# Kernel optimization log

Hardware: AMD Instinct MI355X
Metric: run time of the kernel (lower is better)

Reference implementation:

```python
import jax, jax.numpy as jnp
import numpy as np
import math

IN_CH = 256
EMBED = 128


def setup_inputs() -> dict:
    key = jax.random.key(0)
    k1, k2, k3, k4, k5 = jax.random.split(key, 5)
    N, C, H, W = 4, IN_CH, 64, 64
    x = jax.random.normal(k1, (N, C, H, W), dtype=jnp.float32)
    # conv1x1 weights stored as [out_ch, in_ch] (kernel is 1x1)
    W_qkv = jax.random.normal(k2, (3 * EMBED, C), dtype=jnp.float32) * (1.0 / math.sqrt(C))
    b_qkv = jax.random.normal(k3, (3 * EMBED,), dtype=jnp.float32) * 0.01
    W_out = jax.random.normal(k4, (C, EMBED), dtype=jnp.float32) * (1.0 / math.sqrt(EMBED))
    b_out = jax.random.normal(k5, (C,), dtype=jnp.float32) * 0.01
    return {"x": x, "W_qkv": W_qkv, "b_qkv": b_qkv, "W_out": W_out, "b_out": b_out}


def reference(x, W_qkv, b_qkv, W_out, b_out):
    N, C, H, W = x.shape
    E = EMBED
    HW = H * W
    # conv1x1 QKV projection: (N, 3E, H, W)
    qkv = jnp.einsum('nchw,oc->nohw', x, W_qkv) + b_qkv[None, :, None, None]
    # faithful RAW C-order reshape (N, 3E, H, W) -> (N, HW, 3E), as in torch .reshape
    qkv = qkv.reshape(N, HW, 3 * E)
    q, k, v = jnp.split(qkv, 3, axis=-1)  # each (N, HW, E)
    # scores scaled by 1/sqrt(H*W), softmax over dim=-2 (columns)
    scores = jnp.einsum('nid,njd->nij', q, k) / math.sqrt(HW)
    soft = jax.nn.softmax(scores, axis=-2)
    out = jnp.einsum('nij,njd->nid', soft, v)  # (N, HW, E)
    # faithful RAW C-order reshape (N, HW, E) -> (N, E, H, W)
    out = out.reshape(N, E, H, W)
    # conv1x1 output projection
    y = jnp.einsum('nehw,ce->nchw', out, W_out) + b_out[None, :, None, None]
    return y
```

## Files before the change

### kernel.cpp

```cpp
#include <hip/hip_runtime.h>
#include <hip/hip_bf16.h>


typedef short bfrag __attribute__((ext_vector_type(8)));
typedef float ffrag __attribute__((ext_vector_type(4)));
typedef unsigned short us4 __attribute__((ext_vector_type(4)));
#define MFMA(a,b,c) __builtin_amdgcn_mfma_f32_16x16x32_bf16((a),(b),(c),0,0,0)

__device__ __forceinline__ unsigned short f2bf(float f){
  union { float f; unsigned u; } v; v.f = f;
  unsigned r = v.u + 0x7fffu + ((v.u >> 16) & 1u);
  return (unsigned short)(r >> 16);
}
__device__ __forceinline__ float bf2f(unsigned short h){
  union { unsigned u; float f; } v; v.u = ((unsigned)h) << 16; return v.f;
}
__device__ __forceinline__ unsigned bfpack(float a, float b){
  return (unsigned)f2bf(a) | ((unsigned)f2bf(b) << 16);
}

__global__ __launch_bounds__(256) void k_qkv(const float* __restrict__ x, const float* __restrict__ Wq,
                                             const float* __restrict__ bq, unsigned short* __restrict__ qkv){
  constexpr int LD = 136;
  __shared__ __align__(16) unsigned short As[128*LD];
  __shared__ __align__(16) unsigned short Bs[64*LD];
  char* BsB = (char*)Bs;
  const int o0 = blockIdx.x*128, h0 = blockIdx.y*64, n = blockIdx.z;
  const int t = threadIdx.x, w = t>>6, lane = t&63, lr = lane&15, q4 = lane>>4;
  ffrag acc[8] = {};
  for (int kh = 0; kh < 2; ++kh) {
    __syncthreads();
    #pragma unroll
    for (int r=0;r<8;++r){
      int pi = t + 256*r; int o = pi>>4, seg = pi&15;
      const float* wsrc = Wq + (size_t)(o0+o)*256 + kh*128 + seg*8;
      float4 w0 = *(const float4*)(wsrc);
      float4 w1 = *(const float4*)(wsrc+4);
      us4 lo, hv;
      lo.x=f2bf(w0.x); lo.y=f2bf(w0.y); lo.z=f2bf(w0.z); lo.w=f2bf(w0.w);
      hv.x=f2bf(w1.x); hv.y=f2bf(w1.y); hv.z=f2bf(w1.z); hv.w=f2bf(w1.w);
      *(us4*)&As[o*LD + seg*8]     = lo;
      *(us4*)&As[o*LD + seg*8 + 4] = hv;
    }
    #pragma unroll
    for (int r=0;r<8;++r){
      int idx = t + 256*r; int cl = idx>>4, h4 = idx&15;
      float4 v = *(const float4*)(x + (size_t)(n*256 + kh*128 + cl)*4096 + h0 + h4*4);
      float vv[4] = {v.x, v.y, v.z, v.w};
      #pragma unroll
      for (int u=0;u<4;++u){
        int row = h4*4+u;
        *(unsigned short*)(BsB + row*272 + ((2*cl) ^ (((row>>3)&7)<<4))) = f2bf(vv[u]);
      }
    }
    __syncthreads();
    const int arow = w*16+lr;
    const int akey = ((arow>>3)&7)<<4;
    #pragma unroll
    for (int kk=0;kk<4;++kk){
      bfrag a = *(const bfrag*)(BsB + arow*272 + ((kk*64 + q4*16) ^ akey));
      #pragma unroll
      for (int ot=0;ot<8;++ot){
        bfrag b = *(const bfrag*)&As[(ot*16+lr)*LD + kk*32 + q4*8];
        acc[ot] = MFMA(a,b,acc[ot]);
      }
    }
  }
  size_t base = (size_t)n*384*4096;
  #pragma unroll
  for (int ot=0;ot<8;++ot){
    int o  = o0 + ot*16 + lr;
    float bias = bq[o];
    int hw = h0 + w*16 + q4*4;
    us4 pk;
    pk.x = f2bf(acc[ot][0] + bias); pk.y = f2bf(acc[ot][1] + bias);
    pk.z = f2bf(acc[ot][2] + bias); pk.w = f2bf(acc[ot][3] + bias);
    *(us4*)(qkv + base + (size_t)o*4096 + hw) = pk;
  }
}

__global__ __launch_bounds__(256, 2) void k_stats(const unsigned short* __restrict__ qkv,
                                                  float* __restrict__ zp){
  constexpr int LD = 136;
  __shared__ __align__(16) unsigned short Qs[2][64*LD];
  const int j0 = blockIdx.x*256, ic = blockIdx.y, n = blockIdx.z;
  const int t = threadIdx.x, w = t>>6, lane = t&63, lr = lane&15, q4 = lane>>4;
  size_t base = (size_t)n*384*4096;
  bfrag kf[4][4];
  #pragma unroll
  for (int js=0; js<4; ++js){
    const unsigned short* krow = qkv + base + (size_t)(j0 + w*64 + js*16 + lr)*384 + 128;
    #pragma unroll
    for (int kk=0;kk<4;++kk) kf[js][kk] = *(const bfrag*)(krow + kk*32 + q4*8);
  }
  const int il = t>>4, seg = t&15;
  {
    const int i0 = (ic<<9);
    #pragma unroll
    for (int r=0;r<4;++r)
      *(uint4*)&Qs[0][(il+16*r)*LD + seg*8] =
        *(const uint4*)(qkv + base + (size_t)(i0+il+16*r)*384 + seg*8);
  }
  __syncthreads();
  float Zc[16] = {};
  const float inv64 = 0.015625f;
  for (int rnd=0; rnd<8; ++rnd){
    const int cur = rnd&1;
    uint4 qr[4];
    if (rnd<7){
      const int i1 = (ic<<9) + (rnd+1)*64;
      #pragma unroll
      for (int r=0;r<4;++r)
        qr[r] = *(const uint4*)(qkv + base + (size_t)(i1+il+16*r)*384 + seg*8);
    }
    const unsigned short* qs = Qs[cur];
    #pragma unroll
    for (int it=0; it<4; ++it){
      bfrag qb[4];
      #pragma unroll
      for (int kk=0;kk<4;++kk) qb[kk] = *(const bfrag*)&qs[(it*16+lr)*LD + kk*32 + q4*8];
      #pragma unroll
      for (int js=0; js<4; ++js){
        ffrag s = {};
        #pragma unroll
        for (int kk=0;kk<4;++kk) s = MFMA(kf[js][kk], qb[kk], s);
        #pragma unroll
        for (int r=0;r<4;++r) Zc[js*4+r] += __expf(s[r]*inv64);
      }
    }
    if (rnd<7){
      #pragma unroll
      for (int r=0;r<4;++r) *(uint4*)&Qs[cur^1][(il+16*r)*LD + seg*8] = qr[r];
      __syncthreads();
    }
  }
  #pragma unroll
  for (int v=0; v<16; ++v){
    float z = Zc[v];
    z += __shfl_xor(z, 1); z += __shfl_xor(z, 2);
    z += __shfl_xor(z, 4); z += __shfl_xor(z, 8);
    Zc[v] = z;
  }
  if (lr == 0){
    int jb = j0 + w*64;
    float* zrow = zp + (size_t)((n<<3)+ic)*4096;
    #pragma unroll
    for (int js=0; js<4; ++js)
      #pragma unroll
      for (int r=0;r<4;++r)
        zrow[jb + js*16 + q4*4 + r] = Zc[js*4+r];
  }
}

__global__ __launch_bounds__(256) void k_vtrans(const unsigned short* __restrict__ qkv,
                                                const float* __restrict__ zp,
                                                unsigned short* __restrict__ vt){
  constexpr int LD = 136;
  __shared__ __align__(16) unsigned short T[64*LD];
  __shared__ float invZ[64];
  const int p0 = blockIdx.x*64, n = blockIdx.y;
  const int t = threadIdx.x;
  size_t base = (size_t)n*384*4096;
  #pragma unroll
  for (int r=0;r<4;++r){
    int pi = t + 256*r; int pl = pi>>4, seg = pi&15;
    *(uint4*)&T[pl*LD + seg*8] = *(const uint4*)(qkv + base + (size_t)(p0+pl)*384 + 256 + seg*8);
  }
  if (t < 64){
    float Z = 0.f;
    #pragma unroll
    for (int c=0;c<8;++c) Z += zp[(size_t)((n<<3)+c)*4096 + p0 + t];
    invZ[t] = 1.0f / Z;
  }
  __syncthreads();
  unsigned* vt32 = (unsigned*)(vt + (size_t)n*128*4096);
  #pragma unroll
  for (int r=0;r<16;++r){
    int pi = t + 256*r;
    int d = pi>>5, k = pi&31;
    float lo = bf2f(T[(2*k)*LD + d])   * invZ[2*k];
    float hi = bf2f(T[(2*k+1)*LD + d]) * invZ[2*k+1];
    vt32[(size_t)d*2048 + (p0>>1) + k] = bfpack(lo, hi);
  }
}

__global__ __launch_bounds__(256, 2) void k_attn(const unsigned short* __restrict__ qkv,
                                                 const unsigned short* __restrict__ vtg_all,
                                                 unsigned short* __restrict__ part){
  constexpr int LDK = 136, LDV = 72;
  __shared__ __align__(16) unsigned short Ks[2][64*LDK];
  __shared__ __align__(16) unsigned short Vt[2][128*LDV];
  const int i0 = blockIdx.x*128, jh = blockIdx.y, n = blockIdx.z;
  const int t = threadIdx.x, w = t>>6, lane = t&63, lr = lane&15, q4 = lane>>4;
  size_t base = (size_t)n*384*4096;
  const unsigned short* vtg = vtg_all + (size_t)n*128*4096;
  bfrag qf[2][4];
  #pragma unroll
  for (int isub=0;isub<2;++isub){
    const unsigned short* qrow = qkv + base + (size_t)(i0 + w*32 + isub*16 + lr)*384;
    #pragma unroll
    for (int kk=0;kk<4;++kk) qf[isub][kk] = *(const bfrag*)(qrow + kk*32 + q4*8);
  }
  ffrag acc[8][2] = {};
  const float inv64 = 0.015625f;

  const int jl_k = t>>4, seg_k = t&15;
  const int d_v  = t>>3, c_v  = t&7;
  const int sl0 = lr + 16*((2*q4)   & 3);
  const int sl1 = lr + 16*((2*q4+1) & 3);

  {
    const int j0 = jh*1024;
    #pragma unroll
    for (int r=0;r<4;++r)
      *(uint4*)&Ks[0][(jl_k+16*r)*LDK + seg_k*8] =
        *(const uint4*)(qkv + base + (size_t)(j0 + jl_k + 16*r)*384 + 128 + seg_k*8);
    #pragma unroll
    for (int r=0;r<4;++r)
      *(uint4*)&Vt[0][(d_v+32*r)*LDV + c_v*8] =
        *(const uint4*)(vtg + (size_t)(d_v + 32*r)*4096 + j0 + c_v*8);
  }
  __syncthreads();

  for (int it=0; it<16; ++it){
    const int cur = it & 1;
    uint4 kr[4], vr[4];
    if (it < 15){
      const int jn = jh*1024 + (it+1)*64;
      #pragma unroll
      for (int r=0;r<4;++r)
        kr[r] = *(const uint4*)(qkv + base + (size_t)(jn + jl_k + 16*r)*384 + 128 + seg_k*8);
      #pragma unroll
      for (int r=0;r<4;++r)
        vr[r] = *(const uint4*)(vtg + (size_t)(d_v + 32*r)*4096 + jn + c_v*8);
    }
    unsigned pk[4][2][2];
    #pragma unroll
    for (int jt=0;jt<4;++jt){
      bfrag kf[4];
      #pragma unroll
      for (int kk=0;kk<4;++kk) kf[kk] = *(const bfrag*)&Ks[cur][(jt*16+lr)*LDK + kk*32 + q4*8];
      #pragma unroll
      for (int isub=0;isub<2;++isub){
        ffrag s = {};
        #pragma unroll
        for (int kk=0;kk<4;++kk) s = MFMA(kf[kk], qf[isub][kk], s);
        pk[jt][isub][0] = bfpack(__expf(s[0]*inv64), __expf(s[1]*inv64));
        pk[jt][isub][1] = bfpack(__expf(s[2]*inv64), __expf(s[3]*inv64));
      }
    }
    #pragma unroll
    for (int jk=0;jk<2;++jk){
      union { bfrag b; uint4 u; } pf0, pf1;
      unsigned v0[4], v1[4];
      #pragma unroll
      for (int m=0;m<4;++m){
        const int sl = (m<2) ? sl0 : sl1;
        unsigned a0 = __shfl(pk[2*jk  ][0][m&1], sl);
        unsigned b0 = __shfl(pk[2*jk+1][0][m&1], sl);
        v0[m] = (q4 >= 2) ? b0 : a0;
        unsigned a1 = __shfl(pk[2*jk  ][1][m&1], sl);
        unsigned b1 = __shfl(pk[2*jk+1][1][m&1], sl);
        v1[m] = (q4 >= 2) ? b1 : a1;
      }
      pf0.u = make_uint4(v0[0],v0[1],v0[2],v0[3]);
      pf1.u = make_uint4(v1[0],v1[1],v1[2],v1[3]);
      #pragma unroll
      for (int dt=0;dt<8;++dt){
        bfrag af = *(const bfrag*)&Vt[cur][(dt*16+lr)*LDV + jk*32 + q4*8];
        acc[dt][0] = MFMA(af, pf0.b, acc[dt][0]);
        acc[dt][1] = MFMA(af, pf1.b, acc[dt][1]);
      }
    }
    if (it < 15){
      #pragma unroll
      for (int r=0;r<4;++r) *(uint4*)&Ks[cur^1][(jl_k+16*r)*LDK + seg_k*8] = kr[r];
      #pragma unroll
      for (int r=0;r<4;++r) *(uint4*)&Vt[cur^1][(d_v+32*r)*LDV + c_v*8] = vr[r];
      __syncthreads();
    }
  }
  unsigned short* po = part + (size_t)(jh*4+n)*524288;
  #pragma unroll
  for (int isub=0;isub<2;++isub){
    const int i = i0 + w*32 + isub*16 + lr;
    #pragma unroll
    for (int dt=0;dt<8;++dt){
      us4 pko;
      pko.x = f2bf(acc[dt][isub][0]); pko.y = f2bf(acc[dt][isub][1]);
      pko.z = f2bf(acc[dt][isub][2]); pko.w = f2bf(acc[dt][isub][3]);
      *(us4*)(po + (size_t)i*128 + dt*16 + q4*4) = pko;
    }
  }
}

__global__ __launch_bounds__(256) void k_oproj(const unsigned short* __restrict__ part,
                                               const float* __restrict__ Wo,
                                               const float* __restrict__ bo, float* __restrict__ y){
  constexpr int LD = 136;
  __shared__ __align__(16) unsigned short As[128*LD];
  __shared__ __align__(16) unsigned short Rt[64*LD];
  char* RtB = (char*)Rt;
  const int c0 = blockIdx.x*128, h0 = blockIdx.y*64, n = blockIdx.z;
  const int t = threadIdx.x, w = t>>6, lane = t&63, lr = lane&15, q4 = lane>>4;
  #pragma unroll
  for (int r=0;r<8;++r){
    int pi = t + 256*r; int cl = pi>>4, seg = pi&15;
    const float* wsrc = Wo + (size_t)(c0+cl)*128 + seg*8;
    float4 w0 = *(const float4*)(wsrc);
    float4 w1 = *(const float4*)(wsrc+4);
    us4 lo, hv;
    lo.x=f2bf(w0.x); lo.y=f2bf(w0.y); lo.z=f2bf(w0.z); lo.w=f2bf(w0.w);
    hv.x=f2bf(w1.x); hv.y=f2bf(w1.y); hv.z=f2bf(w1.z); hv.w=f2bf(w1.w);
    *(us4*)&As[cl*LD + seg*8]     = lo;
    *(us4*)&As[cl*LD + seg*8 + 4] = hv;
  }
  #pragma unroll
  for (int r=0;r<4;++r){
    int pi = t + 256*r; int e = pi>>3, h8 = pi&7;
    size_t f = (size_t)e*4096 + h0 + h8*8;
    float a[8] = {};
    #pragma unroll
    for (int s=0;s<4;++s){
      uint4 u = *(const uint4*)(part + (size_t)(s*4+n)*524288 + f);
      a[0] += bf2f((unsigned short)(u.x & 0xffffu)); a[1] += bf2f((unsigned short)(u.x >> 16));
      a[2] += bf2f((unsigned short)(u.y & 0xffffu)); a[3] += bf2f((unsigned short)(u.y >> 16));
      a[4] += bf2f((unsigned short)(u.z & 0xffffu)); a[5] += bf2f((unsigned short)(u.z >> 16));
      a[6] += bf2f((unsigned short)(u.w & 0xffffu)); a[7] += bf2f((unsigned short)(u.w >> 16));
    }
    #pragma unroll
    for (int u2=0;u2<8;++u2){
      int row = h8*8+u2;
      *(unsigned short*)(RtB + row*272 + ((2*e) ^ (((row>>3)&7)<<4))) = f2bf(a[u2]);
    }
  }
  __syncthreads();
  ffrag acc[8] = {};
  const int arow = w*16+lr;
  const int akey = ((arow>>3)&7)<<4;
  #pragma unroll
  for (int kk=0;kk<4;++kk){
    bfrag a = *(const bfrag*)(RtB + arow*272 + ((kk*64 + q4*16) ^ akey));
    #pragma unroll
    for (int cs=0;cs<8;++cs){
      bfrag b = *(const bfrag*)&As[(cs*16+lr)*LD + kk*32 + q4*8];
      acc[cs] = MFMA(a,b,acc[cs]);
    }
  }
  #pragma unroll
  for (int cs=0;cs<8;++cs){
    int c = c0 + cs*16 + lr;
    float bias = bo[c];
    float4 v4 = { acc[cs][0]+bias, acc[cs][1]+bias, acc[cs][2]+bias, acc[cs][3]+bias };
    *(float4*)(y + ((size_t)n*256 + c)*4096 + h0 + w*16 + q4*4) = v4;
  }
}

extern "C" void kernel_launch(void* const* d_in, const int* in_sizes, int n_in,
                              void* d_out, int out_size, void* d_ws, size_t ws_size,
                              hipStream_t stream){
  const float* x  = (const float*)d_in[0];
  const float* Wq = (const float*)d_in[1];
  const float* bq = (const float*)d_in[2];
  const float* Wo = (const float*)d_in[3];
  const float* bo = (const float*)d_in[4];
  float* y = (float*)d_out;
  char* ws = (char*)d_ws;
  unsigned short* qkv  = (unsigned short*)(ws + 0);
  unsigned short* vtg  = (unsigned short*)(ws + 12582912);
  float* zp   = (float*)(ws + 17039360);
  unsigned short* part = (unsigned short*)(ws + 17629184);

  k_qkv   <<<dim3(3,64,4),  256, 0, stream>>>(x, Wq, bq, qkv);
  k_stats <<<dim3(16,8,4),  256, 0, stream>>>(qkv, zp);
  k_vtrans<<<dim3(64,4),    256, 0, stream>>>(qkv, zp, vtg);
  k_attn  <<<dim3(32,4,4),  256, 0, stream>>>(qkv, vtg, part);
  k_oproj <<<dim3(2,64,4),  256, 0, stream>>>(part, Wo, bo, y);
}
```

Before: 182.2 us.

## Fuse five attention stages into one persistent kernel with grid barriers

Replaces five separate kernel launches (QKV projection, softmax column stats, V transpose/normalize, attention, output projection) with a single persistent kernel of 512 blocks. The stages are separated by atomic-counter grid barriers, and a memset resets the counter before launch. This removes per-launch overhead and the idle gaps between kernels. In exchange it needs all 512 blocks to be co-resident, with 2 blocks per CU on 256 CUs and 70KB of shared memory each, or it deadlocks. It also loses occupancy on the lighter stages and adds barrier spin cost.

```diff
diff --git a/kernel.cpp b/kernel.cpp
--- a/kernel.cpp
+++ b/kernel.cpp
@@ -19,340 +19,349 @@
   return (unsigned)f2bf(a) | ((unsigned)f2bf(b) << 16);
 }
 
-__global__ __launch_bounds__(256) void k_qkv(const float* __restrict__ x, const float* __restrict__ Wq,
-                                             const float* __restrict__ bq, unsigned short* __restrict__ qkv){
+__device__ __forceinline__ void grid_barrier(unsigned* bar, unsigned target){
+  __syncthreads();
+  __threadfence();
+  if (threadIdx.x == 0){
+    atomicAdd(bar, 1u);
+    while (__hip_atomic_load(bar, __ATOMIC_RELAXED, __HIP_MEMORY_SCOPE_AGENT) < target)
+      __builtin_amdgcn_s_sleep(2);
+  }
+  __syncthreads();
+  __threadfence();
+}
+
+__global__ __launch_bounds__(256, 2) void k_fused(
+    const float* __restrict__ x,  const float* __restrict__ Wq, const float* __restrict__ bq,
+    const float* __restrict__ Wo, const float* __restrict__ bo,
+    unsigned short* __restrict__ qkv, unsigned short* __restrict__ vtg_all,
+    float* __restrict__ zp, unsigned short* __restrict__ part, float* __restrict__ y,
+    unsigned* __restrict__ bar)
+{
+  __shared__ __align__(16) char smem[71680];
+  const int bid = blockIdx.x;
+  const int t = threadIdx.x, w = t>>6, lane = t&63, lr = lane&15, q4 = lane>>4;
   constexpr int LD = 136;
-  __shared__ __align__(16) unsigned short As[128*LD];
-  __shared__ __align__(16) unsigned short Bs[64*LD];
-  char* BsB = (char*)Bs;
-  const int o0 = blockIdx.x*128, h0 = blockIdx.y*64, n = blockIdx.z;
-  const int t = threadIdx.x, w = t>>6, lane = t&63, lr = lane&15, q4 = lane>>4;
-  ffrag acc[8] = {};
-  for (int kh = 0; kh < 2; ++kh) {
+  const float inv64 = 0.015625f;
+
+  {
+    unsigned short* As = (unsigned short*)smem;
+    char* BsB = smem + 34816;
+    for (int v = bid; v < 768; v += 512){
+      const int o0=(v%3)*128, h0=((v/3)&63)*64, n=v/192;
+      ffrag acc[8] = {};
+      for (int kh = 0; kh < 2; ++kh) {
+        __syncthreads();
+        #pragma unroll
+        for (int r=0;r<8;++r){
+          int pi = t + 256*r; int o = pi>>4, seg = pi&15;
+          const float* wsrc = Wq + (size_t)(o0+o)*256 + kh*128 + seg*8;
+          float4 w0 = *(const float4*)(wsrc);
+          float4 w1 = *(const float4*)(wsrc+4);
+          us4 lo, hv;
+          lo.x=f2bf(w0.x); lo.y=f2bf(w0.y); lo.z=f2bf(w0.z); lo.w=f2bf(w0.w);
+          hv.x=f2bf(w1.x); hv.y=f2bf(w1.y); hv.z=f2bf(w1.z); hv.w=f2bf(w1.w);
+          *(us4*)&As[o*LD + seg*8]     = lo;
+          *(us4*)&As[o*LD + seg*8 + 4] = hv;
+        }
+        #pragma unroll
+        for (int r=0;r<8;++r){
+          int idx = t + 256*r; int cl = idx>>4, h4 = idx&15;
+          float4 v4 = *(const float4*)(x + (size_t)(n*256 + kh*128 + cl)*4096 + h0 + h4*4);
+          float vv[4] = {v4.x, v4.y, v4.z, v4.w};
+          #pragma unroll
+          for (int u=0;u<4;++u){
+            int row = h4*4+u;
+            *(unsigned short*)(BsB + row*272 + ((2*cl) ^ (((row>>3)&7)<<4))) = f2bf(vv[u]);
+          }
+        }
+        __syncthreads();
+        const int arow = w*16+lr;
+        const int akey = ((arow>>3)&7)<<4;
+        #pragma unroll
+        for (int kk=0;kk<4;++kk){
+          bfrag a = *(const bfrag*)(BsB + arow*272 + ((kk*64 + q4*16) ^ akey));
+          #pragma unroll
+          for (int ot=0;ot<8;++ot){
+            bfrag b = *(const bfrag*)&As[(ot*16+lr)*LD + kk*32 + q4*8];
+            acc[ot] = MFMA(a,b,acc[ot]);
+          }
+        }
+      }
+      size_t base = (size_t)n*384*4096;
+      #pragma unroll
+      for (int ot=0;ot<8;++ot){
+        int o  = o0 + ot*16 + lr;
+        float bias = bq[o];
+        int hw = h0 + w*16 + q4*4;
+        us4 pk;
+        pk.x = f2bf(acc[ot][0] + bias); pk.y = f2bf(acc[ot][1] + bias);
+        pk.z = f2bf(acc[ot][2] + bias); pk.w = f2bf(acc[ot][3] + bias);
+        *(us4*)(qkv + base + (size_t)o*4096 + hw) = pk;
+      }
+    }
+  }
+  grid_barrier(bar, 512u);
+
+  {
+    unsigned short (*Qs)[64*LD] = (unsigned short(*)[64*LD])smem;
+    const int j0 = (bid&15)*256, ic = (bid>>4)&7, n = bid>>7;
+    size_t base = (size_t)n*384*4096;
+    bfrag kf[4][4];
+    #pragma unroll
+    for (int js=0; js<4; ++js){
+      const unsigned short* krow = qkv + base + (size_t)(j0 + w*64 + js*16 + lr)*384 + 128;
+      #pragma unroll
+      for (int kk=0;kk<4;++kk) kf[js][kk] = *(const bfrag*)(krow + kk*32 + q4*8);
+    }
+    const int il = t>>4, seg = t&15;
+    {
+      const int i0 = (ic<<9);
+      #pragma unroll
+      for (int r=0;r<4;++r)
+        *(uint4*)&Qs[0][(il+16*r)*LD + seg*8] =
+          *(const uint4*)(qkv + base + (size_t)(i0+il+16*r)*384 + seg*8);
+    }
     __syncthreads();
+    float Zc[16] = {};
+    for (int rnd=0; rnd<8; ++rnd){
+      const int cur = rnd&1;
+      uint4 qr[4];
+      if (rnd<7){
+        const int i1 = (ic<<9) + (rnd+1)*64;
+        #pragma unroll
+        for (int r=0;r<4;++r)
+          qr[r] = *(const uint4*)(qkv + base + (size_t)(i1+il+16*r)*384 + seg*8);
+      }
+      const unsigned short* qs = Qs[cur];
+      #pragma unroll
+      for (int it=0; it<4; ++it){
+        bfrag qb[4];
+        #pragma unroll
+        for (int kk=0;kk<4;++kk) qb[kk] = *(const bfrag*)&qs[(it*16+lr)*LD + kk*32 + q4*8];
+        #pragma unroll
+        for (int js=0; js<4; ++js){
+          ffrag s = {};
+          #pragma unroll
+          for (int kk=0;kk<4;++kk) s = MFMA(kf[js][kk], qb[kk], s);
+          #pragma unroll
+          for (int r=0;r<4;++r) Zc[js*4+r] += __expf(s[r]*inv64);
+        }
+      }
+      if (rnd<7){
+        #pragma unroll
+        for (int r=0;r<4;++r) *(uint4*)&Qs[cur^1][(il+16*r)*LD + seg*8] = qr[r];
+        __syncthreads();
+      }
+    }
+    #pragma unroll
+    for (int v=0; v<16; ++v){
+      float z = Zc[v];
+      z += __shfl_xor(z, 1); z += __shfl_xor(z, 2);
+      z += __shfl_xor(z, 4); z += __shfl_xor(z, 8);
+      Zc[v] = z;
+    }
+    if (lr == 0){
+      int jb = j0 + w*64;
+      float* zrow = zp + (size_t)((n<<3)+ic)*4096;
+      #pragma unroll
+      for (int js=0; js<4; ++js)
+        #pragma unroll
+        for (int r=0;r<4;++r)
+          zrow[jb + js*16 + q4*4 + r] = Zc[js*4+r];
+    }
+  }
+  grid_barrier(bar, 1024u);
+
+  if (bid < 256){
+    unsigned short* T = (unsigned short*)smem;
+    float* invZ = (float*)(smem + 17408);
+    const int p0 = (bid&63)*64, n = bid>>6;
+    size_t base = (size_t)n*384*4096;
+    #pragma unroll
+    for (int r=0;r<4;++r){
+      int pi = t + 256*r; int pl = pi>>4, seg = pi&15;
+      *(uint4*)&T[pl*LD + seg*8] = *(const uint4*)(qkv + base + (size_t)(p0+pl)*384 + 256 + seg*8);
+    }
+    if (t < 64){
+      float Z = 0.f;
+      #pragma unroll
+      for (int c=0;c<8;++c) Z += zp[(size_t)((n<<3)+c)*4096 + p0 + t];
+      invZ[t] = 1.0f / Z;
+    }
+    __syncthreads();
+    unsigned* vt32 = (unsigned*)(vtg_all + (size_t)n*128*4096);
+    #pragma unroll
+    for (int r=0;r<16;++r){
+      int pi = t + 256*r;
+      int d = pi>>5, k = pi&31;
+      float lo = bf2f(T[(2*k)*LD + d])   * invZ[2*k];
+      float hi = bf2f(T[(2*k+1)*LD + d]) * invZ[2*k+1];
+      vt32[(size_t)d*2048 + (p0>>1) + k] = bfpack(lo, hi);
+    }
+  }
+  grid_barrier(bar, 1536u);
+
+  {
+    constexpr int LDK = 136, LDV = 72;
+    unsigned short (*Ks)[64*LDK] = (unsigned short(*)[64*LDK])smem;
+    unsigned short (*Vt)[128*LDV] = (unsigned short(*)[128*LDV])(smem + 34816);
+    const int i0 = (bid&31)*128, jh = (bid>>5)&3, n = bid>>7;
+    size_t base = (size_t)n*384*4096;
+    const unsigned short* vtg = vtg_all + (size_t)n*128*4096;
+    bfrag qf[2][4];
+    #pragma unroll
+    for (int isub=0;isub<2;++isub){
+      const unsigned short* qrow = qkv + base + (size_t)(i0 + w*32 + isub*16 + lr)*384;
+      #pragma unroll
+      for (int kk=0;kk<4;++kk) qf[isub][kk] = *(const bfrag*)(qrow + kk*32 + q4*8);
+    }
+    ffrag acc[8][2] = {};
+    const int jl_k = t>>4, seg_k = t&15;
+    const int d_v  = t>>3, c_v  = t&7;
+    const int sl0 = lr + 16*((2*q4)   & 3);
+    const int sl1 = lr + 16*((2*q4+1) & 3);
+    {
+      const int j0 = jh*1024;
+      #pragma unroll
+      for (int r=0;r<4;++r)
+        *(uint4*)&Ks[0][(jl_k+16*r)*LDK + seg_k*8] =
+          *(const uint4*)(qkv + base + (size_t)(j0 + jl_k + 16*r)*384 + 128 + seg_k*8);
+      #pragma unroll
+      for (int r=0;r<4;++r)
+        *(uint4*)&Vt[0][(d_v+32*r)*LDV + c_v*8] =
+          *(const uint4*)(vtg + (size_t)(d_v + 32*r)*4096 + j0 + c_v*8);
+    }
+    __syncthreads();
+
+    for (int it=0; it<16; ++it){
+      const int cur = it & 1;
+      uint4 kr[4], vr[4];
+      if (it < 15){
+        const int jn = jh*1024 + (it+1)*64;
+        #pragma unroll
+        for (int r=0;r<4;++r)
+          kr[r] = *(const uint4*)(qkv + base + (size_t)(jn + jl_k + 16*r)*384 + 128 + seg_k*8);
+        #pragma unroll
+        for (int r=0;r<4;++r)
+          vr[r] = *(const uint4*)(vtg + (size_t)(d_v + 32*r)*4096 + jn + c_v*8);
+      }
+      unsigned pk[4][2][2];
+      #pragma unroll
+      for (int jt=0;jt<4;++jt){
+        bfrag kf[4];
+        #pragma unroll
+        for (int kk=0;kk<4;++kk) kf[kk] = *(const bfrag*)&Ks[cur][(jt*16+lr)*LDK + kk*32 + q4*8];
+        #pragma unroll
+        for (int isub=0;isub<2;++isub){
+          ffrag s = {};
+          #pragma unroll
+          for (int kk=0;kk<4;++kk) s = MFMA(kf[kk], qf[isub][kk], s);
+          pk[jt][isub][0] = bfpack(__expf(s[0]*inv64), __expf(s[1]*inv64));
+          pk[jt][isub][1] = bfpack(__expf(s[2]*inv64), __expf(s[3]*inv64));
+        }
+      }
+      #pragma unroll
+      for (int jk=0;jk<2;++jk){
+        union { bfrag b; uint4 u; } pf0, pf1;
+        unsigned v0[4], v1[4];
+        #pragma unroll
+        for (int m=0;m<4;++m){
+          const int sl = (m<2) ? sl0 : sl1;
+          unsigned a0 = __shfl(pk[2*jk  ][0][m&1], sl);
+          unsigned b0 = __shfl(pk[2*jk+1][0][m&1], sl);
+          v0[m] = (q4 >= 2) ? b0 : a0;
+          unsigned a1 = __shfl(pk[2*jk  ][1][m&1], sl);
+          unsigned b1 = __shfl(pk[2*jk+1][1][m&1], sl);
+          v1[m] = (q4 >= 2) ? b1 : a1;
+        }
+        pf0.u = make_uint4(v0[0],v0[1],v0[2],v0[3]);
+        pf1.u = make_uint4(v1[0],v1[1],v1[2],v1[3]);
+        #pragma unroll
+        for (int dt=0;dt<8;++dt){
+          bfrag af = *(const bfrag*)&Vt[cur][(dt*16+lr)*LDV + jk*32 + q4*8];
+          acc[dt][0] = MFMA(af, pf0.b, acc[dt][0]);
+          acc[dt][1] = MFMA(af, pf1.b, acc[dt][1]);
+        }
+      }
+      if (it < 15){
+        #pragma unroll
+        for (int r=0;r<4;++r) *(uint4*)&Ks[cur^1][(jl_k+16*r)*LDK + seg_k*8] = kr[r];
+        #pragma unroll
+        for (int r=0;r<4;++r) *(uint4*)&Vt[cur^1][(d_v+32*r)*LDV + c_v*8] = vr[r];
+        __syncthreads();
+      }
+    }
+    unsigned short* po = part + (size_t)(jh*4+n)*524288;
+    #pragma unroll
+    for (int isub=0;isub<2;++isub){
+      const int i = i0 + w*32 + isub*16 + lr;
+      #pragma unroll
+      for (int dt=0;dt<8;++dt){
+        us4 pko;
+        pko.x = f2bf(acc[dt][isub][0]); pko.y = f2bf(acc[dt][isub][1]);
+        pko.z = f2bf(acc[dt][isub][2]); pko.w = f2bf(acc[dt][isub][3]);
+        *(us4*)(po + (size_t)i*128 + dt*16 + q4*4) = pko;
+      }
+    }
+  }
+  grid_barrier(bar, 2048u);
+
+  {
+    unsigned short* As = (unsigned short*)smem;
+    char* RtB = smem + 34816;
+    const int c0 = (bid&1)*128, h0 = ((bid>>1)&63)*64, n = bid>>7;
     #pragma unroll
     for (int r=0;r<8;++r){
-      int pi = t + 256*r; int o = pi>>4, seg = pi&15;
-      const float* wsrc = Wq + (size_t)(o0+o)*256 + kh*128 + seg*8;
+      int pi = t + 256*r; int cl = pi>>4, seg = pi&15;
+      const float* wsrc = Wo + (size_t)(c0+cl)*128 + seg*8;
       float4 w0 = *(const float4*)(wsrc);
       float4 w1 = *(const float4*)(wsrc+4);
       us4 lo, hv;
       lo.x=f2bf(w0.x); lo.y=f2bf(w0.y); lo.z=f2bf(w0.z); lo.w=f2bf(w0.w);
       hv.x=f2bf(w1.x); hv.y=f2bf(w1.y); hv.z=f2bf(w1.z); hv.w=f2bf(w1.w);
-      *(us4*)&As[o*LD + seg*8]     = lo;
-      *(us4*)&As[o*LD + seg*8 + 4] = hv;
-    }
-    #pragma unroll
-    for (int r=0;r<8;++r){
-      int idx = t + 256*r; int cl = idx>>4, h4 = idx&15;
-      float4 v = *(const float4*)(x + (size_t)(n*256 + kh*128 + cl)*4096 + h0 + h4*4);
-      float vv[4] = {v.x, v.y, v.z, v.w};
-      #pragma unroll
-      for (int u=0;u<4;++u){
-        int row = h4*4+u;
-        *(unsigned short*)(BsB + row*272 + ((2*cl) ^ (((row>>3)&7)<<4))) = f2bf(vv[u]);
+      *(us4*)&As[cl*LD + seg*8]     = lo;
+      *(us4*)&As[cl*LD + seg*8 + 4] = hv;
+    }
+    #pragma unroll
+    for (int r=0;r<4;++r){
+      int pi = t + 256*r; int e = pi>>3, h8 = pi&7;
+      size_t f = (size_t)e*4096 + h0 + h8*8;
+      float a[8] = {};
+      #pragma unroll
+      for (int s=0;s<4;++s){
+        uint4 u = *(const uint4*)(part + (size_t)(s*4+n)*524288 + f);
+        a[0] += bf2f((unsigned short)(u.x & 0xffffu)); a[1] += bf2f((unsigned short)(u.x >> 16));
+        a[2] += bf2f((unsigned short)(u.y & 0xffffu)); a[3] += bf2f((unsigned short)(u.y >> 16));
+        a[4] += bf2f((unsigned short)(u.z & 0xffffu)); a[5] += bf2f((unsigned short)(u.z >> 16));
+        a[6] += bf2f((unsigned short)(u.w & 0xffffu)); a[7] += bf2f((unsigned short)(u.w >> 16));
+      }
+      #pragma unroll
+      for (int u2=0;u2<8;++u2){
+        int row = h8*8+u2;
+        *(unsigned short*)(RtB + row*272 + ((2*e) ^ (((row>>3)&7)<<4))) = f2bf(a[u2]);
       }
     }
     __syncthreads();
+    ffrag acc[8] = {};
     const int arow = w*16+lr;
     const int akey = ((arow>>3)&7)<<4;
     #pragma unroll
     for (int kk=0;kk<4;++kk){
-      bfrag a = *(const bfrag*)(BsB + arow*272 + ((kk*64 + q4*16) ^ akey));
-      #pragma unroll
-      for (int ot=0;ot<8;++ot){
-        bfrag b = *(const bfrag*)&As[(ot*16+lr)*LD + kk*32 + q4*8];
-        acc[ot] = MFMA(a,b,acc[ot]);
-      }
-    }
-  }
-  size_t base = (size_t)n*384*4096;
-  #pragma unroll
-  for (int ot=0;ot<8;++ot){
-    int o  = o0 + ot*16 + lr;
-    float bias = bq[o];
-    int hw = h0 + w*16 + q4*4;
-    us4 pk;
-    pk.x = f2bf(acc[ot][0] + bias); pk.y = f2bf(acc[ot][1] + bias);
-    pk.z = f2bf(acc[ot][2] + bias); pk.w = f2bf(acc[ot][3] + bias);
-    *(us4*)(qkv + base + (size_t)o*4096 + hw) = pk;
-  }
-}
-
-__global__ __launch_bounds__(256, 2) void k_stats(const unsigned short* __restrict__ qkv,
-                                                  float* __restrict__ zp){
-  constexpr int LD = 136;
-  __shared__ __align__(16) unsigned short Qs[2][64*LD];
-  const int j0 = blockIdx.x*256, ic = blockIdx.y, n = blockIdx.z;
-  const int t = threadIdx.x, w = t>>6, lane = t&63, lr = lane&15, q4 = lane>>4;
-  size_t base = (size_t)n*384*4096;
-  bfrag kf[4][4];
-  #pragma unroll
-  for (int js=0; js<4; ++js){
-    const unsigned short* krow = qkv + base + (size_t)(j0 + w*64 + js*16 + lr)*384 + 128;
-    #pragma unroll
-    for (int kk=0;kk<4;++kk) kf[js][kk] = *(const bfrag*)(krow + kk*32 + q4*8);
-  }
-  const int il = t>>4, seg = t&15;
-  {
-    const int i0 = (ic<<9);
-    #pragma unroll
-    for (int r=0;r<4;++r)
-      *(uint4*)&Qs[0][(il+16*r)*LD + seg*8] =
-        *(const uint4*)(qkv + base + (size_t)(i0+il+16*r)*384 + seg*8);
-  }
-  __syncthreads();
-  float Zc[16] = {};
-  const float inv64 = 0.015625f;
-  for (int rnd=0; rnd<8; ++rnd){
-    const int cur = rnd&1;
-    uint4 qr[4];
-    if (rnd<7){
-      const int i1 = (ic<<9) + (rnd+1)*64;
-      #pragma unroll
-      for (int r=0;r<4;++r)
-        qr[r] = *(const uint4*)(qkv + base + (size_t)(i1+il+16*r)*384 + seg*8);
-    }
-    const unsigned short* qs = Qs[cur];
-    #pragma unroll
-    for (int it=0; it<4; ++it){
-      bfrag qb[4];
-      #pragma unroll
-      for (int kk=0;kk<4;++kk) qb[kk] = *(const bfrag*)&qs[(it*16+lr)*LD + kk*32 + q4*8];
-      #pragma unroll
-      for (int js=0; js<4; ++js){
-        ffrag s = {};
-        #pragma unroll
-        for (int kk=0;kk<4;++kk) s = MFMA(kf[js][kk], qb[kk], s);
-        #pragma unroll
-        for (int r=0;r<4;++r) Zc[js*4+r] += __expf(s[r]*inv64);
-      }
-    }
-    if (rnd<7){
-      #pragma unroll
-      for (int r=0;r<4;++r) *(uint4*)&Qs[cur^1][(il+16*r)*LD + seg*8] = qr[r];
-      __syncthreads();
-    }
-  }
-  #pragma unroll
-  for (int v=0; v<16; ++v){
-    float z = Zc[v];
-    z += __shfl_xor(z, 1); z += __shfl_xor(z, 2);
-    z += __shfl_xor(z, 4); z += __shfl_xor(z, 8);
-    Zc[v] = z;
-  }
-  if (lr == 0){
-    int jb = j0 + w*64;
-    float* zrow = zp + (size_t)((n<<3)+ic)*4096;
-    #pragma unroll
-    for (int js=0; js<4; ++js)
-      #pragma unroll
-      for (int r=0;r<4;++r)
-        zrow[jb + js*16 + q4*4 + r] = Zc[js*4+r];
-  }
-}
-
-__global__ __launch_bounds__(256) void k_vtrans(const unsigned short* __restrict__ qkv,
-                                                const float* __restrict__ zp,
-                                                unsigned short* __restrict__ vt){
-  constexpr int LD = 136;
-  __shared__ __align__(16) unsigned short T[64*LD];
-  __shared__ float invZ[64];
-  const int p0 = blockIdx.x*64, n = blockIdx.y;
-  const int t = threadIdx.x;
-  size_t base = (size_t)n*384*4096;
-  #pragma unroll
-  for (int r=0;r<4;++r){
-    int pi = t + 256*r; int pl = pi>>4, seg = pi&15;
-    *(uint4*)&T[pl*LD + seg*8] = *(const uint4*)(qkv + base + (size_t)(p0+pl)*384 + 256 + seg*8);
-  }
-  if (t < 64){
-    float Z = 0.f;
-    #pragma unroll
-    for (int c=0;c<8;++c) Z += zp[(size_t)((n<<3)+c)*4096 + p0 + t];
-    invZ[t] = 1.0f / Z;
-  }
-  __syncthreads();
-  unsigned* vt32 = (unsigned*)(vt + (size_t)n*128*4096);
-  #pragma unroll
-  for (int r=0;r<16;++r){
-    int pi = t + 256*r;
-    int d = pi>>5, k = pi&31;
-    float lo = bf2f(T[(2*k)*LD + d])   * invZ[2*k];
-    float hi = bf2f(T[(2*k+1)*LD + d]) * invZ[2*k+1];
-    vt32[(size_t)d*2048 + (p0>>1) + k] = bfpack(lo, hi);
-  }
-}
-
-__global__ __launch_bounds__(256, 2) void k_attn(const unsigned short* __restrict__ qkv,
-                                                 const unsigned short* __restrict__ vtg_all,
-                                                 unsigned short* __restrict__ part){
-  constexpr int LDK = 136, LDV = 72;
-  __shared__ __align__(16) unsigned short Ks[2][64*LDK];
-  __shared__ __align__(16) unsigned short Vt[2][128*LDV];
-  const int i0 = blockIdx.x*128, jh = blockIdx.y, n = blockIdx.z;
-  const int t = threadIdx.x, w = t>>6, lane = t&63, lr = lane&15, q4 = lane>>4;
-  size_t base = (size_t)n*384*4096;
-  const unsigned short* vtg = vtg_all + (size_t)n*128*4096;
-  bfrag qf[2][4];
-  #pragma unroll
-  for (int isub=0;isub<2;++isub){
-    const unsigned short* qrow = qkv + base + (size_t)(i0 + w*32 + isub*16 + lr)*384;
-    #pragma unroll
-    for (int kk=0;kk<4;++kk) qf[isub][kk] = *(const bfrag*)(qrow + kk*32 + q4*8);
-  }
-  ffrag acc[8][2] = {};
-  const float inv64 = 0.015625f;
-
-  const int jl_k = t>>4, seg_k = t&15;
-  const int d_v  = t>>3, c_v  = t&7;
-  const int sl0 = lr + 16*((2*q4)   & 3);
-  const int sl1 = lr + 16*((2*q4+1) & 3);
-
-  {
-    const int j0 = jh*1024;
-    #pragma unroll
-    for (int r=0;r<4;++r)
-      *(uint4*)&Ks[0][(jl_k+16*r)*LDK + seg_k*8] =
-        *(const uint4*)(qkv + base + (size_t)(j0 + jl_k + 16*r)*384 + 128 + seg_k*8);
-    #pragma unroll
-    for (int r=0;r<4;++r)
-      *(uint4*)&Vt[0][(d_v+32*r)*LDV + c_v*8] =
-        *(const uint4*)(vtg + (size_t)(d_v + 32*r)*4096 + j0 + c_v*8);
-  }
-  __syncthreads();
-
-  for (int it=0; it<16; ++it){
-    const int cur = it & 1;
-    uint4 kr[4], vr[4];
-    if (it < 15){
-      const int jn = jh*1024 + (it+1)*64;
-      #pragma unroll
-      for (int r=0;r<4;++r)
-        kr[r] = *(const uint4*)(qkv + base + (size_t)(jn + jl_k + 16*r)*384 + 128 + seg_k*8);
-      #pragma unroll
-      for (int r=0;r<4;++r)
-        vr[r] = *(const uint4*)(vtg + (size_t)(d_v + 32*r)*4096 + jn + c_v*8);
-    }
-    unsigned pk[4][2][2];
-    #pragma unroll
-    for (int jt=0;jt<4;++jt){
-      bfrag kf[4];
-      #pragma unroll
-      for (int kk=0;kk<4;++kk) kf[kk] = *(const bfrag*)&Ks[cur][(jt*16+lr)*LDK + kk*32 + q4*8];
-      #pragma unroll
-      for (int isub=0;isub<2;++isub){
-        ffrag s = {};
-        #pragma unroll
-        for (int kk=0;kk<4;++kk) s = MFMA(kf[kk], qf[isub][kk], s);
-        pk[jt][isub][0] = bfpack(__expf(s[0]*inv64), __expf(s[1]*inv64));
-        pk[jt][isub][1] = bfpack(__expf(s[2]*inv64), __expf(s[3]*inv64));
-      }
-    }
-    #pragma unroll
-    for (int jk=0;jk<2;++jk){
-      union { bfrag b; uint4 u; } pf0, pf1;
-      unsigned v0[4], v1[4];
-      #pragma unroll
-      for (int m=0;m<4;++m){
-        const int sl = (m<2) ? sl0 : sl1;
-        unsigned a0 = __shfl(pk[2*jk  ][0][m&1], sl);
-        unsigned b0 = __shfl(pk[2*jk+1][0][m&1], sl);
-        v0[m] = (q4 >= 2) ? b0 : a0;
-        unsigned a1 = __shfl(pk[2*jk  ][1][m&1], sl);
-        unsigned b1 = __shfl(pk[2*jk+1][1][m&1], sl);
-        v1[m] = (q4 >= 2) ? b1 : a1;
-      }
-      pf0.u = make_uint4(v0[0],v0[1],v0[2],v0[3]);
-      pf1.u = make_uint4(v1[0],v1[1],v1[2],v1[3]);
-      #pragma unroll
-      for (int dt=0;dt<8;++dt){
-        bfrag af = *(const bfrag*)&Vt[cur][(dt*16+lr)*LDV + jk*32 + q4*8];
-        acc[dt][0] = MFMA(af, pf0.b, acc[dt][0]);
-        acc[dt][1] = MFMA(af, pf1.b, acc[dt][1]);
-      }
-    }
-    if (it < 15){
-      #pragma unroll
-      for (int r=0;r<4;++r) *(uint4*)&Ks[cur^1][(jl_k+16*r)*LDK + seg_k*8] = kr[r];
-      #pragma unroll
-      for (int r=0;r<4;++r) *(uint4*)&Vt[cur^1][(d_v+32*r)*LDV + c_v*8] = vr[r];
-      __syncthreads();
-    }
-  }
-  unsigned short* po = part + (size_t)(jh*4+n)*524288;
-  #pragma unroll
-  for (int isub=0;isub<2;++isub){
-    const int i = i0 + w*32 + isub*16 + lr;
-    #pragma unroll
-    for (int dt=0;dt<8;++dt){
-      us4 pko;
-      pko.x = f2bf(acc[dt][isub][0]); pko.y = f2bf(acc[dt][isub][1]);
-      pko.z = f2bf(acc[dt][isub][2]); pko.w = f2bf(acc[dt][isub][3]);
-      *(us4*)(po + (size_t)i*128 + dt*16 + q4*4) = pko;
-    }
-  }
-}
-
-__global__ __launch_bounds__(256) void k_oproj(const unsigned short* __restrict__ part,
-                                               const float* __restrict__ Wo,
-                                               const float* __restrict__ bo, float* __restrict__ y){
-  constexpr int LD = 136;
-  __shared__ __align__(16) unsigned short As[128*LD];
-  __shared__ __align__(16) unsigned short Rt[64*LD];
-  char* RtB = (char*)Rt;
-  const int c0 = blockIdx.x*128, h0 = blockIdx.y*64, n = blockIdx.z;
-  const int t = threadIdx.x, w = t>>6, lane = t&63, lr = lane&15, q4 = lane>>4;
-  #pragma unroll
-  for (int r=0;r<8;++r){
-    int pi = t + 256*r; int cl = pi>>4, seg = pi&15;
-    const float* wsrc = Wo + (size_t)(c0+cl)*128 + seg*8;
-    float4 w0 = *(const float4*)(wsrc);
-    float4 w1 = *(const float4*)(wsrc+4);
-    us4 lo, hv;
-    lo.x=f2bf(w0.x); lo.y=f2bf(w0.y); lo.z=f2bf(w0.z); lo.w=f2bf(w0.w);
-    hv.x=f2bf(w1.x); hv.y=f2bf(w1.y); hv.z=f2bf(w1.z); hv.w=f2bf(w1.w);
-    *(us4*)&As[cl*LD + seg*8]     = lo;
-    *(us4*)&As[cl*LD + seg*8 + 4] = hv;
-  }
-  #pragma unroll
-  for (int r=0;r<4;++r){
-    int pi = t + 256*r; int e = pi>>3, h8 = pi&7;
-    size_t f = (size_t)e*4096 + h0 + h8*8;
-    float a[8] = {};
-    #pragma unroll
-    for (int s=0;s<4;++s){
-      uint4 u = *(const uint4*)(part + (size_t)(s*4+n)*524288 + f);
-      a[0] += bf2f((unsigned short)(u.x & 0xffffu)); a[1] += bf2f((unsigned short)(u.x >> 16));
-      a[2] += bf2f((unsigned short)(u.y & 0xffffu)); a[3] += bf2f((unsigned short)(u.y >> 16));
-      a[4] += bf2f((unsigned short)(u.z & 0xffffu)); a[5] += bf2f((unsigned short)(u.z >> 16));
-      a[6] += bf2f((unsigned short)(u.w & 0xffffu)); a[7] += bf2f((unsigned short)(u.w >> 16));
-    }
-    #pragma unroll
-    for (int u2=0;u2<8;++u2){
-      int row = h8*8+u2;
-      *(unsigned short*)(RtB + row*272 + ((2*e) ^ (((row>>3)&7)<<4))) = f2bf(a[u2]);
-    }
-  }
-  __syncthreads();
-  ffrag acc[8] = {};
-  const int arow = w*16+lr;
-  const int akey = ((arow>>3)&7)<<4;
-  #pragma unroll
-  for (int kk=0;kk<4;++kk){
-    bfrag a = *(const bfrag*)(RtB + arow*272 + ((kk*64 + q4*16) ^ akey));
+      bfrag a = *(const bfrag*)(RtB + arow*272 + ((kk*64 + q4*16) ^ akey));
+      #pragma unroll
+      for (int cs=0;cs<8;++cs){
+        bfrag b = *(const bfrag*)&As[(cs*16+lr)*LD + kk*32 + q4*8];
+        acc[cs] = MFMA(a,b,acc[cs]);
+      }
+    }
     #pragma unroll
     for (int cs=0;cs<8;++cs){
-      bfrag b = *(const bfrag*)&As[(cs*16+lr)*LD + kk*32 + q4*8];
-      acc[cs] = MFMA(a,b,acc[cs]);
-    }
-  }
-  #pragma unroll
-  for (int cs=0;cs<8;++cs){
-    int c = c0 + cs*16 + lr;
-    float bias = bo[c];
-    float4 v4 = { acc[cs][0]+bias, acc[cs][1]+bias, acc[cs][2]+bias, acc[cs][3]+bias };
-    *(float4*)(y + ((size_t)n*256 + c)*4096 + h0 + w*16 + q4*4) = v4;
+      int c = c0 + cs*16 + lr;
+      float bias = bo[c];
+      float4 v4 = { acc[cs][0]+bias, acc[cs][1]+bias, acc[cs][2]+bias, acc[cs][3]+bias };
+      *(float4*)(y + ((size_t)n*256 + c)*4096 + h0 + w*16 + q4*4) = v4;
+    }
   }
 }
 
@@ -369,11 +378,9 @@
   unsigned short* qkv  = (unsigned short*)(ws + 0);
   unsigned short* vtg  = (unsigned short*)(ws + 12582912);
   float* zp   = (float*)(ws + 17039360);
+  unsigned* bar = (unsigned*)(ws + 17563648);
   unsigned short* part = (unsigned short*)(ws + 17629184);
 
-  k_qkv   <<<dim3(3,64,4),  256, 0, stream>>>(x, Wq, bq, qkv);
-  k_stats <<<dim3(16,8,4),  256, 0, stream>>>(qkv, zp);
-  k_vtrans<<<dim3(64,4),    256, 0, stream>>>(qkv, zp, vtg);
-  k_attn  <<<dim3(32,4,4),  256, 0, stream>>>(qkv, vtg, part);
-  k_oproj <<<dim3(2,64,4),  256, 0, stream>>>(part, Wo, bo, y);
-}
+  hipMemsetAsync(bar, 0, 64, stream);
+  k_fused<<<dim3(512), dim3(256), 0, stream>>>(x, Wq, bq, Wo, bo, qkv, vtg, zp, part, y, bar);
+}
```

Result: slower. 653.3 us (+258.5%).

## Load Q and K fragments directly from global memory instead of LDS staging

Applied to the files above, without the earlier changes.

Removes the LDS double-buffered staging of Q tiles in the stats kernel and K tiles in the attention kernel. MFMA fragments are now read straight from global memory, relying on L2/L1 caching. This cuts LDS traffic and footprint, and drops the barriers in the stats kernel. In exchange each wave issues uncoalesced-ish global loads without software prefetch, so load latency may no longer be hidden.

```diff
diff --git a/kernel.cpp b/kernel.cpp
--- a/kernel.cpp
+++ b/kernel.cpp
@@ -81,8 +81,6 @@
 
 __global__ __launch_bounds__(256, 2) void k_stats(const unsigned short* __restrict__ qkv,
                                                   float* __restrict__ zp){
-  constexpr int LD = 136;
-  __shared__ __align__(16) unsigned short Qs[2][64*LD];
   const int j0 = blockIdx.x*256, ic = blockIdx.y, n = blockIdx.z;
   const int t = threadIdx.x, w = t>>6, lane = t&63, lr = lane&15, q4 = lane>>4;
   size_t base = (size_t)n*384*4096;
@@ -93,32 +91,16 @@
     #pragma unroll
     for (int kk=0;kk<4;++kk) kf[js][kk] = *(const bfrag*)(krow + kk*32 + q4*8);
   }
-  const int il = t>>4, seg = t&15;
-  {
-    const int i0 = (ic<<9);
-    #pragma unroll
-    for (int r=0;r<4;++r)
-      *(uint4*)&Qs[0][(il+16*r)*LD + seg*8] =
-        *(const uint4*)(qkv + base + (size_t)(i0+il+16*r)*384 + seg*8);
-  }
-  __syncthreads();
   float Zc[16] = {};
   const float inv64 = 0.015625f;
   for (int rnd=0; rnd<8; ++rnd){
-    const int cur = rnd&1;
-    uint4 qr[4];
-    if (rnd<7){
-      const int i1 = (ic<<9) + (rnd+1)*64;
-      #pragma unroll
-      for (int r=0;r<4;++r)
-        qr[r] = *(const uint4*)(qkv + base + (size_t)(i1+il+16*r)*384 + seg*8);
-    }
-    const unsigned short* qs = Qs[cur];
+    const int i0 = (ic<<9) + rnd*64;
     #pragma unroll
     for (int it=0; it<4; ++it){
       bfrag qb[4];
-      #pragma unroll
-      for (int kk=0;kk<4;++kk) qb[kk] = *(const bfrag*)&qs[(it*16+lr)*LD + kk*32 + q4*8];
+      const unsigned short* qrow = qkv + base + (size_t)(i0 + it*16 + lr)*384;
+      #pragma unroll
+      for (int kk=0;kk<4;++kk) qb[kk] = *(const bfrag*)(qrow + kk*32 + q4*8);
       #pragma unroll
       for (int js=0; js<4; ++js){
         ffrag s = {};
@@ -127,11 +109,6 @@
         #pragma unroll
         for (int r=0;r<4;++r) Zc[js*4+r] += __expf(s[r]*inv64);
       }
-    }
-    if (rnd<7){
-      #pragma unroll
-      for (int r=0;r<4;++r) *(uint4*)&Qs[cur^1][(il+16*r)*LD + seg*8] = qr[r];
-      __syncthreads();
     }
   }
   #pragma unroll
@@ -187,8 +164,7 @@
 __global__ __launch_bounds__(256, 2) void k_attn(const unsigned short* __restrict__ qkv,
                                                  const unsigned short* __restrict__ vtg_all,
                                                  unsigned short* __restrict__ part){
-  constexpr int LDK = 136, LDV = 72;
-  __shared__ __align__(16) unsigned short Ks[2][64*LDK];
+  constexpr int LDV = 72;
   __shared__ __align__(16) unsigned short Vt[2][128*LDV];
   const int i0 = blockIdx.x*128, jh = blockIdx.y, n = blockIdx.z;
   const int t = threadIdx.x, w = t>>6, lane = t&63, lr = lane&15, q4 = lane>>4;
@@ -204,7 +180,6 @@
   ffrag acc[8][2] = {};
   const float inv64 = 0.015625f;
 
-  const int jl_k = t>>4, seg_k = t&15;
   const int d_v  = t>>3, c_v  = t&7;
   const int sl0 = lr + 16*((2*q4)   & 3);
   const int sl1 = lr + 16*((2*q4+1) & 3);
@@ -213,10 +188,6 @@
     const int j0 = jh*1024;
     #pragma unroll
     for (int r=0;r<4;++r)
-      *(uint4*)&Ks[0][(jl_k+16*r)*LDK + seg_k*8] =
-        *(const uint4*)(qkv + base + (size_t)(j0 + jl_k + 16*r)*384 + 128 + seg_k*8);
-    #pragma unroll
-    for (int r=0;r<4;++r)
       *(uint4*)&Vt[0][(d_v+32*r)*LDV + c_v*8] =
         *(const uint4*)(vtg + (size_t)(d_v + 32*r)*4096 + j0 + c_v*8);
   }
@@ -224,12 +195,10 @@
 
   for (int it=0; it<16; ++it){
     const int cur = it & 1;
-    uint4 kr[4], vr[4];
+    const int j0 = jh*1024 + it*64;
+    uint4 vr[4];
     if (it < 15){
-      const int jn = jh*1024 + (it+1)*64;
-      #pragma unroll
-      for (int r=0;r<4;++r)
-        kr[r] = *(const uint4*)(qkv + base + (size_t)(jn + jl_k + 16*r)*384 + 128 + seg_k*8);
+      const int jn = j0 + 64;
       #pragma unroll
       for (int r=0;r<4;++r)
         vr[r] = *(const uint4*)(vtg + (size_t)(d_v + 32*r)*4096 + jn + c_v*8);
@@ -238,8 +207,9 @@
     #pragma unroll
     for (int jt=0;jt<4;++jt){
       bfrag kf[4];
-      #pragma unroll
-      for (int kk=0;kk<4;++kk) kf[kk] = *(const bfrag*)&Ks[cur][(jt*16+lr)*LDK + kk*32 + q4*8];
+      const unsigned short* krow = qkv + base + (size_t)(j0 + jt*16 + lr)*384 + 128;
+      #pragma unroll
+      for (int kk=0;kk<4;++kk) kf[kk] = *(const bfrag*)(krow + kk*32 + q4*8);
       #pragma unroll
       for (int isub=0;isub<2;++isub){
         ffrag s = {};
@@ -273,8 +243,6 @@
       }
     }
     if (it < 15){
-      #pragma unroll
-      for (int r=0;r<4;++r) *(uint4*)&Ks[cur^1][(jl_k+16*r)*LDK + seg_k*8] = kr[r];
       #pragma unroll
       for (int r=0;r<4;++r) *(uint4*)&Vt[cur^1][(d_v+32*r)*LDV + c_v*8] = vr[r];
       __syncthreads();
```

New measurement: 236.9 us. +30.0%, slower.
